# Kernel tuning notes

Hardware: AMD Instinct MI355X
Metric: run time of the kernel (lower is better)

Reference implementation:

```python
import jax, jax.numpy as jnp
import numpy as np

B, LS, LL = 1024, 128, 2048
E, VOCAB = 16, 160000
NH, KD = 8, 6
LSH_DIM, TOPK = 16, 48
D_ITEM = 3 * E  # 48
EPS = 1e-3  # keras LayerNormalization default epsilon


def setup_inputs() -> dict:
    key = jax.random.key(0)
    ks = iter(jax.random.split(key, 64))
    def nk():
        return next(ks)
    def ids(shape):
        return jax.random.randint(nk(), shape, 0, VOCAB, dtype=jnp.int32)
    inp = {}
    for n in ['uid', 'utag1', 'utag2', 'utag3', 'utag4',
              'label_goods_ids', 'label_shop_ids', 'label_cate_ids']:
        inp[n] = ids((B,))
    for n in ['shortterm_goods_ids', 'shortterm_shop_ids', 'shortterm_cate_ids']:
        inp[n] = ids((B, LS))
    for n in ['longterm_goods_ids', 'longterm_shop_ids', 'longterm_cate_ids']:
        inp[n] = ids((B, LL))
    def rn(shape, s=0.05):
        return (jax.random.normal(nk(), shape) * s).astype(jnp.float32)
    inp['emb_table'] = rn((VOCAB, E))
    inp['H'] = rn((D_ITEM, LSH_DIM), 1.0)  # non-trainable random projection
    for p in ('s', 'l'):
        inp[p + 'Wq'] = rn((D_ITEM, NH, KD)); inp[p + 'bq'] = jnp.zeros((NH, KD), jnp.float32)
        inp[p + 'Wk'] = rn((D_ITEM, NH, KD)); inp[p + 'bk'] = jnp.zeros((NH, KD), jnp.float32)
        inp[p + 'Wv'] = rn((D_ITEM, NH, KD)); inp[p + 'bv'] = jnp.zeros((NH, KD), jnp.float32)
        inp[p + 'Wo'] = rn((NH, KD, D_ITEM)); inp[p + 'bo'] = jnp.zeros((D_ITEM,), jnp.float32)
    Din = D_ITEM + 5 * E + D_ITEM + D_ITEM  # 224
    inp['W1'] = rn((Din, 200)); inp['b1'] = jnp.zeros((200,), jnp.float32)
    inp['g1'] = jnp.ones((200,), jnp.float32); inp['be1'] = jnp.zeros((200,), jnp.float32)
    inp['W2'] = rn((200, 80)); inp['b2'] = jnp.zeros((80,), jnp.float32)
    inp['g2'] = jnp.ones((80,), jnp.float32); inp['be2'] = jnp.zeros((80,), jnp.float32)
    inp['W3'] = rn((80, 1)); inp['b3'] = jnp.zeros((1,), jnp.float32)
    return inp


def _ln(x, g, b):
    m = jnp.mean(x, axis=-1, keepdims=True)
    v = jnp.mean((x - m) ** 2, axis=-1, keepdims=True)
    return (x - m) * jax.lax.rsqrt(v + EPS) * g + b


def _mha(q, kv, mask3, Wq, bq, Wk, bk, Wv, bv, Wo, bo):
    # q: [B,1,D], kv: [B,K,D], mask3: [B,1,K] float (1=keep)
    qh = jnp.einsum('bqe,ehd->bqhd', q, Wq) + bq
    kh = jnp.einsum('bke,ehd->bkhd', kv, Wk) + bk
    vh = jnp.einsum('bke,ehd->bkhd', kv, Wv) + bv
    sc = jnp.einsum('bqhd,bkhd->bhqk', qh, kh) / jnp.sqrt(jnp.float32(KD))
    sc = sc + (1.0 - mask3[:, None, :, :]) * jnp.float32(-1e9)
    a = jax.nn.softmax(sc, axis=-1)
    o = jnp.einsum('bhqk,bkhd->bqhd', a, vh)
    return jnp.einsum('bqhd,hde->bqe', o, Wo) + bo


def reference(uid, utag1, utag2, utag3, utag4,
              label_goods_ids, label_shop_ids, label_cate_ids,
              shortterm_goods_ids, shortterm_shop_ids, shortterm_cate_ids,
              longterm_goods_ids, longterm_shop_ids, longterm_cate_ids,
              emb_table, H,
              sWq, sbq, sWk, sbk, sWv, sbv, sWo, sbo,
              lWq, lbq, lWk, lbk, lWv, lbv, lWo, lbo,
              W1, b1, g1, be1, W2, b2, g2, be2, W3, b3):
    short_mask = shortterm_goods_ids == 0  # padding_index == 0
    long_mask = longterm_goods_ids == 0

    def stack_embed(lst):
        X = jnp.stack([t if t.ndim == 2 else t[:, None] for t in lst], axis=2)  # [B,L,F]
        Xe = emb_table[X]  # [B,L,F,E]
        return Xe.reshape(Xe.shape[0], Xe.shape[1], -1)

    X_item = stack_embed([label_goods_ids, label_shop_ids, label_cate_ids])  # [B,1,48]
    X_user = stack_embed([uid, utag1, utag2, utag3, utag4])                  # [B,1,80]
    X_short = stack_embed([shortterm_goods_ids, shortterm_shop_ids, shortterm_cate_ids])  # [B,LS,48]
    X_long = stack_embed([longterm_goods_ids, longterm_shop_ids, longterm_cate_ids])      # [B,LL,48]

    # short-term interest
    slen = jnp.sum((~short_mask).astype(jnp.int32), axis=1)
    smask = (jnp.arange(LS)[None, :] < slen[:, None]).astype(jnp.float32)[:, None, :]
    short_int = _mha(X_item, X_short, smask, sWq, sbq, sWk, sbk, sWv, sbv, sWo, sbo)[:, 0]

    # long-term interest: LSH sign-hash hamming top-k retrieval
    series_codes = jnp.sign(jnp.einsum('ble,em->blm', X_long, H))  # [B,LL,16]
    item_codes = jnp.sign(jnp.einsum('ble,em->blm', X_item, H))    # [B,1,16]
    scores = jnp.sum((series_codes == item_codes).astype(jnp.float32), axis=-1)  # [B,LL]
    scores = jnp.where(long_mask, -jnp.inf, scores)
    _, idx = jax.lax.top_k(scores, TOPK)  # descending, padded entries last
    top_emb = jnp.take_along_axis(X_long, idx[:, :, None], axis=1)  # [B,TOPK,48]
    top_mask = jnp.take_along_axis(long_mask, idx, axis=1)
    llen = jnp.sum((~top_mask).astype(jnp.int32), axis=1)
    lmask = (jnp.arange(TOPK)[None, :] < llen[:, None]).astype(jnp.float32)[:, None, :]
    long_int = _mha(X_item, top_emb, lmask, lWq, lbq, lWk, lbk, lWv, lbv, lWo, lbo)[:, 0]

    x = jnp.concatenate([X_item[:, 0], X_user[:, 0], short_int, long_int], axis=1)  # [B,224]
    h1 = jax.nn.relu(_ln(x @ W1 + b1, g1, be1))
    h2 = jax.nn.relu(_ln(h1 @ W2 + b2, g2, be2))
    out = jax.nn.sigmoid(h2 @ W3 + b3)  # [B,1]
    return out
```

## Files before the change

### kernel.cpp

```cpp
#include <hip/hip_runtime.h>
#include <math.h>

#define BB 1024
#define LSx 128
#define LLx 2048
#define TOPKx 48

__global__ __launch_bounds__(256) void k_score_topk(
    const int* __restrict__ lg, const int* __restrict__ lsh, const int* __restrict__ lc,
    const int* __restrict__ ig, const int* __restrict__ ish, const int* __restrict__ ici,
    const float* __restrict__ emb, const float* __restrict__ Hm,
    int* __restrict__ sel)
{
  __shared__ float Xitem[48];
  __shared__ int icode[16];
  __shared__ signed char scores[LLx];
  __shared__ int hist[18];
  __shared__ int cnt_above;
  __shared__ int wsum[4];
  const int b = blockIdx.x, tid = threadIdx.x;

  if (tid < 48) {
    const int seg = tid >> 4, e = tid & 15;
    const int id = (seg == 0) ? ig[b] : (seg == 1) ? ish[b] : ici[b];
    Xitem[tid] = emb[(size_t)id * 16 + e];
  }
  if (tid < 18) hist[tid] = 0;
  if (tid == 0) cnt_above = 0;
  __syncthreads();
  if (tid < 16) {
    float dd = 0.f;
    for (int e = 0; e < 48; ++e) dd += Xitem[e] * Hm[e * 16 + tid];
    icode[tid] = (dd > 0.f) ? 1 : (dd < 0.f ? -1 : 0);
  }
  __syncthreads();

  for (int j = 0; j < LLx / 256; ++j) {
    const int l = j * 256 + tid;
    const size_t off = (size_t)b * LLx + l;
    const int gid = lg[off];
    int sc;
    if (gid == 0) {
      sc = -1;
    } else {
      const int sid = lsh[off], cid = lc[off];
      float d[16];
      #pragma unroll
      for (int m = 0; m < 16; ++m) d[m] = 0.f;
      const int ids3[3] = {gid, sid, cid};
      #pragma unroll
      for (int seg = 0; seg < 3; ++seg) {
        const float* row = emb + (size_t)ids3[seg] * 16;
        const float4 r0 = ((const float4*)row)[0];
        const float4 r1 = ((const float4*)row)[1];
        const float4 r2 = ((const float4*)row)[2];
        const float4 r3 = ((const float4*)row)[3];
        const float x[16] = {r0.x, r0.y, r0.z, r0.w, r1.x, r1.y, r1.z, r1.w,
                             r2.x, r2.y, r2.z, r2.w, r3.x, r3.y, r3.z, r3.w};
        const float* hb = Hm + seg * 256;
        #pragma unroll
        for (int i = 0; i < 16; ++i) {
          const float xi = x[i];
          #pragma unroll
          for (int mc = 0; mc < 4; ++mc) {
            const float4 h4 = *(const float4*)(hb + i * 16 + mc * 4);
            d[mc * 4 + 0] += xi * h4.x;
            d[mc * 4 + 1] += xi * h4.y;
            d[mc * 4 + 2] += xi * h4.z;
            d[mc * 4 + 3] += xi * h4.w;
          }
        }
      }
      sc = 0;
      #pragma unroll
      for (int m = 0; m < 16; ++m) {
        const int cs = (d[m] > 0.f) ? 1 : (d[m] < 0.f ? -1 : 0);
        sc += (cs == icode[m]) ? 1 : 0;
      }
    }
    scores[l] = (signed char)sc;
    atomicAdd(&hist[sc + 1], 1);
  }
  __syncthreads();

  int above = 0, tval = -1, need = 0;
  for (int s = 16; s >= -1; --s) {
    const int c = hist[s + 1];
    if (above + c >= TOPKx) { tval = s; need = TOPKx - above; break; }
    above += c;
  }

  const int base_l = tid * (LLx / 256);
  int cnt = 0;
  for (int j = 0; j < LLx / 256; ++j) cnt += (scores[base_l + j] == tval) ? 1 : 0;
  int v = cnt;
  const int lane = tid & 63, wave = tid >> 6;
  #pragma unroll
  for (int o = 1; o < 64; o <<= 1) {
    const int u = __shfl_up(v, o, 64);
    if (lane >= o) v += u;
  }
  if (lane == 63) wsum[wave] = v;
  __syncthreads();
  int rank = v - cnt;
  for (int w = 0; w < wave; ++w) rank += wsum[w];

  for (int j = 0; j < LLx / 256; ++j) {
    const int l = base_l + j;
    const int s = scores[l];
    if (s > tval) {
      const int slot = atomicAdd(&cnt_above, 1);
      sel[b * TOPKx + slot] = l;
    } else if (s == tval) {
      if (rank < need) sel[b * TOPKx + above + rank] = l;
      ++rank;
    }
  }
}

template<int K, int STRIDE, bool IS_LONG>
__global__ __launch_bounds__(128) void k_mha(
    const int* __restrict__ kg, const int* __restrict__ ks, const int* __restrict__ kc,
    const int* __restrict__ ig, const int* __restrict__ ish, const int* __restrict__ ici,
    const float* __restrict__ emb,
    const float* __restrict__ Wq, const float* __restrict__ bq,
    const float* __restrict__ Wk, const float* __restrict__ bk,
    const float* __restrict__ Wv, const float* __restrict__ bv,
    const float* __restrict__ Wo, const float* __restrict__ bo,
    const int* __restrict__ sel,
    float* __restrict__ outv)
{
  __shared__ float Xitem[48];
  __shared__ float qh[48];
  __shared__ __align__(16) float vhs[K][48];
  __shared__ float scs[8][K + 4];
  __shared__ float osm[48];
  __shared__ unsigned char validf[K];
  const int b = blockIdx.x, tid = threadIdx.x;

  if (tid < 48) {
    const int seg = tid >> 4, e = tid & 15;
    const int id = (seg == 0) ? ig[b] : (seg == 1) ? ish[b] : ici[b];
    Xitem[tid] = emb[(size_t)id * 16 + e];
  }
  __syncthreads();
  if (tid < 48) {
    float a = bq[tid];
    for (int e = 0; e < 48; ++e) a += Xitem[e] * Wq[e * 48 + tid];
    qh[tid] = a;
  }

  int gid = 0, sid = 0, cid = 0;
  if (tid < K) {
    const int pos = IS_LONG ? sel[b * TOPKx + tid] : tid;
    const size_t off = (size_t)b * STRIDE + pos;
    gid = kg[off]; sid = ks[off]; cid = kc[off];
  }
  const int nval = __syncthreads_count((tid < K) && (gid != 0));

  if (tid < K) {
    validf[tid] = IS_LONG ? (unsigned char)(gid != 0) : (unsigned char)(tid < nval);
    float kh[48], vh[48];
    #pragma unroll
    for (int j = 0; j < 48; ++j) { kh[j] = bk[j]; vh[j] = bv[j]; }
    const int ids3[3] = {gid, sid, cid};
    #pragma unroll
    for (int seg = 0; seg < 3; ++seg) {
      const float* row = emb + (size_t)ids3[seg] * 16;
      #pragma unroll
      for (int i4 = 0; i4 < 4; ++i4) {
        const float4 xv = ((const float4*)row)[i4];
        const float xs[4] = {xv.x, xv.y, xv.z, xv.w};
        #pragma unroll
        for (int c = 0; c < 4; ++c) {
          const int e = seg * 16 + i4 * 4 + c;
          const float* wkr = Wk + e * 48;
          const float* wvr = Wv + e * 48;
          const float xe = xs[c];
          #pragma unroll
          for (int j = 0; j < 48; ++j) {
            kh[j] += xe * wkr[j];
            vh[j] += xe * wvr[j];
          }
        }
      }
    }
    #pragma unroll
    for (int h = 0; h < 8; ++h) {
      float s = 0.f;
      #pragma unroll
      for (int d = 0; d < 6; ++d) s += qh[h * 6 + d] * kh[h * 6 + d];
      scs[h][tid] = s * 0.40824829046386301637f;
    }
    #pragma unroll
    for (int j = 0; j < 48; ++j) vhs[tid][j] = vh[j];
  }
  __syncthreads();

  {
    const int h = tid >> 4, l16 = tid & 15;
    float amax = -INFINITY;
    for (int k = l16; k < K; k += 16) if (validf[k]) amax = fmaxf(amax, scs[h][k]);
    #pragma unroll
    for (int m = 1; m < 16; m <<= 1) amax = fmaxf(amax, __shfl_xor(amax, m, 16));
    if (nval == 0) {
      for (int k = l16; k < K; k += 16) scs[h][k] = 1.0f / (float)K;
    } else {
      float ssum = 0.f;
      for (int k = l16; k < K; k += 16) {
        const float ev = validf[k] ? expf(scs[h][k] - amax) : 0.f;
        scs[h][k] = ev;
        ssum += ev;
      }
      #pragma unroll
      for (int m = 1; m < 16; m <<= 1) ssum += __shfl_xor(ssum, m, 16);
      const float inv = 1.0f / ssum;
      for (int k = l16; k < K; k += 16) scs[h][k] *= inv;
    }
  }
  __syncthreads();

  if (tid < 48) {
    const int h = tid / 6;
    float a = 0.f;
    for (int k = 0; k < K; ++k) a += scs[h][k] * vhs[k][tid];
    osm[tid] = a;
  }
  __syncthreads();
  if (tid < 48) {
    float r = bo[tid];
    for (int j = 0; j < 48; ++j) r += osm[j] * Wo[j * 48 + tid];
    outv[b * 48 + tid] = r;
  }
}

__device__ __forceinline__ float block_sum256(float v, float* red) {
  #pragma unroll
  for (int m = 32; m >= 1; m >>= 1) v += __shfl_xor(v, m, 64);
  const int lane = threadIdx.x & 63, wave = threadIdx.x >> 6;
  if (lane == 0) red[wave] = v;
  __syncthreads();
  const float t = red[0] + red[1] + red[2] + red[3];
  __syncthreads();
  return t;
}

__global__ __launch_bounds__(256) void k_mlp(
    const int* __restrict__ uid, const int* __restrict__ u1, const int* __restrict__ u2,
    const int* __restrict__ u3, const int* __restrict__ u4,
    const int* __restrict__ ig, const int* __restrict__ ish, const int* __restrict__ ici,
    const float* __restrict__ emb,
    const float* __restrict__ sint, const float* __restrict__ lint,
    const float* __restrict__ W1, const float* __restrict__ b1,
    const float* __restrict__ g1, const float* __restrict__ be1,
    const float* __restrict__ W2, const float* __restrict__ b2,
    const float* __restrict__ g2, const float* __restrict__ be2,
    const float* __restrict__ W3, const float* __restrict__ b3,
    float* __restrict__ out)
{
  __shared__ __align__(16) float x[224];
  __shared__ __align__(16) float h1[200];
  __shared__ float h2[80];
  __shared__ float red[4];
  const int b = blockIdx.x, tid = threadIdx.x;

  if (tid < 128) {
    const int e = tid & 15;
    int id;
    if (tid < 48) {
      const int seg = tid >> 4;
      id = (seg == 0) ? ig[b] : (seg == 1) ? ish[b] : ici[b];
    } else {
      const int f = (tid - 48) >> 4;
      id = (f == 0) ? uid[b] : (f == 1) ? u1[b] : (f == 2) ? u2[b] : (f == 3) ? u3[b] : u4[b];
    }
    x[tid] = emb[(size_t)id * 16 + e];
  } else if (tid < 176) {
    x[tid] = sint[b * 48 + (tid - 128)];
  } else if (tid < 224) {
    x[tid] = lint[b * 48 + (tid - 176)];
  }
  __syncthreads();

  float v = 0.f;
  if (tid < 200) {
    v = b1[tid];
    for (int i4 = 0; i4 < 56; ++i4) {
      const float4 xv = *(const float4*)(x + i4 * 4);
      const float* w = W1 + i4 * 4 * 200 + tid;
      v += xv.x * w[0];
      v += xv.y * w[200];
      v += xv.z * w[400];
      v += xv.w * w[600];
    }
  }
  const float mean1 = block_sum256((tid < 200) ? v : 0.f, red) * (1.0f / 200.0f);
  const float dv = (tid < 200) ? (v - mean1) : 0.f;
  const float var1 = block_sum256(dv * dv, red) * (1.0f / 200.0f);
  if (tid < 200) {
    const float y = (v - mean1) * rsqrtf(var1 + 1e-3f) * g1[tid] + be1[tid];
    h1[tid] = fmaxf(y, 0.f);
  }
  __syncthreads();

  float v2 = 0.f;
  if (tid < 80) {
    v2 = b2[tid];
    for (int i4 = 0; i4 < 50; ++i4) {
      const float4 xv = *(const float4*)(h1 + i4 * 4);
      const float* w = W2 + i4 * 4 * 80 + tid;
      v2 += xv.x * w[0];
      v2 += xv.y * w[80];
      v2 += xv.z * w[160];
      v2 += xv.w * w[240];
    }
  }
  const float mean2 = block_sum256((tid < 80) ? v2 : 0.f, red) * (1.0f / 80.0f);
  const float dv2 = (tid < 80) ? (v2 - mean2) : 0.f;
  const float var2 = block_sum256(dv2 * dv2, red) * (1.0f / 80.0f);
  if (tid < 80) {
    const float y = (v2 - mean2) * rsqrtf(var2 + 1e-3f) * g2[tid] + be2[tid];
    h2[tid] = fmaxf(y, 0.f);
  }
  __syncthreads();

  const float p = (tid < 80) ? h2[tid] * W3[tid] : 0.f;
  const float z = block_sum256(p, red);
  if (tid == 0) {
    out[b] = 1.0f / (1.0f + expf(-(z + b3[0])));
  }
}

extern "C" void kernel_launch(void* const* d_in, const int* in_sizes, int n_in,
                              void* d_out, int out_size, void* d_ws, size_t ws_size,
                              hipStream_t stream) {
  (void)in_sizes; (void)n_in; (void)out_size; (void)ws_size;
  const int* uid = (const int*)d_in[0];
  const int* u1  = (const int*)d_in[1];
  const int* u2  = (const int*)d_in[2];
  const int* u3  = (const int*)d_in[3];
  const int* u4  = (const int*)d_in[4];
  const int* ig  = (const int*)d_in[5];
  const int* ish = (const int*)d_in[6];
  const int* ici = (const int*)d_in[7];
  const int* sg  = (const int*)d_in[8];
  const int* ss  = (const int*)d_in[9];
  const int* scd = (const int*)d_in[10];
  const int* lg  = (const int*)d_in[11];
  const int* ls  = (const int*)d_in[12];
  const int* lcd = (const int*)d_in[13];
  const float* emb = (const float*)d_in[14];
  const float* Hm  = (const float*)d_in[15];
  const float* sWq = (const float*)d_in[16];
  const float* sbq = (const float*)d_in[17];
  const float* sWk = (const float*)d_in[18];
  const float* sbk = (const float*)d_in[19];
  const float* sWv = (const float*)d_in[20];
  const float* sbv = (const float*)d_in[21];
  const float* sWo = (const float*)d_in[22];
  const float* sbo = (const float*)d_in[23];
  const float* lWq = (const float*)d_in[24];
  const float* lbq = (const float*)d_in[25];
  const float* lWk = (const float*)d_in[26];
  const float* lbk = (const float*)d_in[27];
  const float* lWv = (const float*)d_in[28];
  const float* lbv = (const float*)d_in[29];
  const float* lWo = (const float*)d_in[30];
  const float* lbo = (const float*)d_in[31];
  const float* W1 = (const float*)d_in[32];
  const float* b1 = (const float*)d_in[33];
  const float* g1 = (const float*)d_in[34];
  const float* be1 = (const float*)d_in[35];
  const float* W2 = (const float*)d_in[36];
  const float* b2 = (const float*)d_in[37];
  const float* g2 = (const float*)d_in[38];
  const float* be2 = (const float*)d_in[39];
  const float* W3 = (const float*)d_in[40];
  const float* b3 = (const float*)d_in[41];
  float* out = (float*)d_out;

  int* sel = (int*)d_ws;
  float* sint = (float*)d_ws + BB * TOPKx;
  float* lint = sint + BB * 48;

  k_score_topk<<<dim3(BB), dim3(256), 0, stream>>>(lg, ls, lcd, ig, ish, ici, emb, Hm, sel);
  k_mha<128, 128, false><<<dim3(BB), dim3(128), 0, stream>>>(
      sg, ss, scd, ig, ish, ici, emb,
      sWq, sbq, sWk, sbk, sWv, sbv, sWo, sbo, (const int*)nullptr, sint);
  k_mha<48, 2048, true><<<dim3(BB), dim3(128), 0, stream>>>(
      lg, ls, lcd, ig, ish, ici, emb,
      lWq, lbq, lWk, lbk, lWv, lbv, lWo, lbo, sel, lint);
  k_mlp<<<dim3(BB), dim3(256), 0, stream>>>(
      uid, u1, u2, u3, u4, ig, ish, ici, emb,
      sint, lint, W1, b1, g1, be1, W2, b2, g2, be2, W3, b3, out);
}
```

Baseline: 337.0 us.

## Split LSH scoring across more blocks and fuse top-k into long MHA

The scoring kernel now launches one block per 256 sequence positions per batch row (8x more blocks), each thread scoring a single position and writing int8 scores to global workspace. Top-k selection (histogram threshold, prefix-rank tie handling) moves into a new long-attention kernel that keeps the selected indices in shared memory and then runs the attention directly. This aims to raise occupancy and parallelism in the gather-heavy scoring stage and to avoid writing and rereading the selected indices. In exchange, each scoring block recomputes the item code, and the scores take a 2MB round trip through global memory.

New measurement: 352.4 us. +4.6%, slower.

```diff
diff --git a/kernel.cpp b/kernel.cpp
--- a/kernel.cpp
+++ b/kernel.cpp
@@ -6,27 +6,21 @@
 #define LLx 2048
 #define TOPKx 48
 
-__global__ __launch_bounds__(256) void k_score_topk(
+__global__ __launch_bounds__(256) void k_score(
     const int* __restrict__ lg, const int* __restrict__ lsh, const int* __restrict__ lc,
     const int* __restrict__ ig, const int* __restrict__ ish, const int* __restrict__ ici,
     const float* __restrict__ emb, const float* __restrict__ Hm,
-    int* __restrict__ sel)
+    signed char* __restrict__ gsc)
 {
   __shared__ float Xitem[48];
   __shared__ int icode[16];
-  __shared__ signed char scores[LLx];
-  __shared__ int hist[18];
-  __shared__ int cnt_above;
-  __shared__ int wsum[4];
-  const int b = blockIdx.x, tid = threadIdx.x;
+  const int b = blockIdx.y, tid = threadIdx.x;
 
   if (tid < 48) {
     const int seg = tid >> 4, e = tid & 15;
     const int id = (seg == 0) ? ig[b] : (seg == 1) ? ish[b] : ici[b];
     Xitem[tid] = emb[(size_t)id * 16 + e];
   }
-  if (tid < 18) hist[tid] = 0;
-  if (tid == 0) cnt_above = 0;
   __syncthreads();
   if (tid < 16) {
     float dd = 0.f;
@@ -35,87 +29,49 @@
   }
   __syncthreads();
 
-  for (int j = 0; j < LLx / 256; ++j) {
-    const int l = j * 256 + tid;
-    const size_t off = (size_t)b * LLx + l;
-    const int gid = lg[off];
-    int sc;
-    if (gid == 0) {
-      sc = -1;
-    } else {
-      const int sid = lsh[off], cid = lc[off];
-      float d[16];
-      #pragma unroll
-      for (int m = 0; m < 16; ++m) d[m] = 0.f;
-      const int ids3[3] = {gid, sid, cid};
-      #pragma unroll
-      for (int seg = 0; seg < 3; ++seg) {
-        const float* row = emb + (size_t)ids3[seg] * 16;
-        const float4 r0 = ((const float4*)row)[0];
-        const float4 r1 = ((const float4*)row)[1];
-        const float4 r2 = ((const float4*)row)[2];
-        const float4 r3 = ((const float4*)row)[3];
-        const float x[16] = {r0.x, r0.y, r0.z, r0.w, r1.x, r1.y, r1.z, r1.w,
-                             r2.x, r2.y, r2.z, r2.w, r3.x, r3.y, r3.z, r3.w};
-        const float* hb = Hm + seg * 256;
+  const int l = blockIdx.x * 256 + tid;
+  const size_t off = (size_t)b * LLx + l;
+  const int gid = lg[off];
+  int sc;
+  if (gid == 0) {
+    sc = -1;
+  } else {
+    const int sid = lsh[off], cid = lc[off];
+    float d[16];
+    #pragma unroll
+    for (int m = 0; m < 16; ++m) d[m] = 0.f;
+    const int ids3[3] = {gid, sid, cid};
+    #pragma unroll
+    for (int seg = 0; seg < 3; ++seg) {
+      const float* row = emb + (size_t)ids3[seg] * 16;
+      const float4 r0 = ((const float4*)row)[0];
+      const float4 r1 = ((const float4*)row)[1];
+      const float4 r2 = ((const float4*)row)[2];
+      const float4 r3 = ((const float4*)row)[3];
+      const float x[16] = {r0.x, r0.y, r0.z, r0.w, r1.x, r1.y, r1.z, r1.w,
+                           r2.x, r2.y, r2.z, r2.w, r3.x, r3.y, r3.z, r3.w};
+      const float* hb = Hm + seg * 256;
+      #pragma unroll
+      for (int i = 0; i < 16; ++i) {
+        const float xi = x[i];
         #pragma unroll
-        for (int i = 0; i < 16; ++i) {
-          const float xi = x[i];
-          #pragma unroll
-          for (int mc = 0; mc < 4; ++mc) {
-            const float4 h4 = *(const float4*)(hb + i * 16 + mc * 4);
-            d[mc * 4 + 0] += xi * h4.x;
-            d[mc * 4 + 1] += xi * h4.y;
-            d[mc * 4 + 2] += xi * h4.z;
-            d[mc * 4 + 3] += xi * h4.w;
-          }
+        for (int mc = 0; mc < 4; ++mc) {
+          const float4 h4 = *(const float4*)(hb + i * 16 + mc * 4);
+          d[mc * 4 + 0] += xi * h4.x;
+          d[mc * 4 + 1] += xi * h4.y;
+          d[mc * 4 + 2] += xi * h4.z;
+          d[mc * 4 + 3] += xi * h4.w;
         }
       }
-      sc = 0;
-      #pragma unroll
-      for (int m = 0; m < 16; ++m) {
-        const int cs = (d[m] > 0.f) ? 1 : (d[m] < 0.f ? -1 : 0);
-        sc += (cs == icode[m]) ? 1 : 0;
-      }
-    }
-    scores[l] = (signed char)sc;
-    atomicAdd(&hist[sc + 1], 1);
-  }
-  __syncthreads();
-
-  int above = 0, tval = -1, need = 0;
-  for (int s = 16; s >= -1; --s) {
-    const int c = hist[s + 1];
-    if (above + c >= TOPKx) { tval = s; need = TOPKx - above; break; }
-    above += c;
-  }
-
-  const int base_l = tid * (LLx / 256);
-  int cnt = 0;
-  for (int j = 0; j < LLx / 256; ++j) cnt += (scores[base_l + j] == tval) ? 1 : 0;
-  int v = cnt;
-  const int lane = tid & 63, wave = tid >> 6;
-  #pragma unroll
-  for (int o = 1; o < 64; o <<= 1) {
-    const int u = __shfl_up(v, o, 64);
-    if (lane >= o) v += u;
-  }
-  if (lane == 63) wsum[wave] = v;
-  __syncthreads();
-  int rank = v - cnt;
-  for (int w = 0; w < wave; ++w) rank += wsum[w];
-
-  for (int j = 0; j < LLx / 256; ++j) {
-    const int l = base_l + j;
-    const int s = scores[l];
-    if (s > tval) {
-      const int slot = atomicAdd(&cnt_above, 1);
-      sel[b * TOPKx + slot] = l;
-    } else if (s == tval) {
-      if (rank < need) sel[b * TOPKx + above + rank] = l;
-      ++rank;
-    }
-  }
+    }
+    sc = 0;
+    #pragma unroll
+    for (int m = 0; m < 16; ++m) {
+      const int cs = (d[m] > 0.f) ? 1 : (d[m] < 0.f ? -1 : 0);
+      sc += (cs == icode[m]) ? 1 : 0;
+    }
+  }
+  gsc[off] = (signed char)sc;
 }
 
 template<int K, int STRIDE, bool IS_LONG>
@@ -224,6 +180,172 @@
     const int h = tid / 6;
     float a = 0.f;
     for (int k = 0; k < K; ++k) a += scs[h][k] * vhs[k][tid];
+    osm[tid] = a;
+  }
+  __syncthreads();
+  if (tid < 48) {
+    float r = bo[tid];
+    for (int j = 0; j < 48; ++j) r += osm[j] * Wo[j * 48 + tid];
+    outv[b * 48 + tid] = r;
+  }
+}
+
+__global__ __launch_bounds__(256) void k_mha_long(
+    const int* __restrict__ kg, const int* __restrict__ ks, const int* __restrict__ kc,
+    const int* __restrict__ ig, const int* __restrict__ ish, const int* __restrict__ ici,
+    const float* __restrict__ emb,
+    const float* __restrict__ Wq, const float* __restrict__ bq,
+    const float* __restrict__ Wk, const float* __restrict__ bk,
+    const float* __restrict__ Wv, const float* __restrict__ bv,
+    const float* __restrict__ Wo, const float* __restrict__ bo,
+    const signed char* __restrict__ gsc,
+    float* __restrict__ outv)
+{
+  __shared__ int hist[18];
+  __shared__ int cnt_above;
+  __shared__ int wsum[4];
+  __shared__ int selsh[TOPKx];
+  __shared__ float Xitem[48];
+  __shared__ float qh[48];
+  __shared__ __align__(16) float vhs[TOPKx][48];
+  __shared__ float scs[8][TOPKx + 4];
+  __shared__ float osm[48];
+  __shared__ unsigned char validf[TOPKx];
+  const int b = blockIdx.x, tid = threadIdx.x;
+
+  const int2 myv = ((const int2*)(gsc + (size_t)b * LLx))[tid];
+  signed char loc[8];
+  *(int2*)loc = myv;
+
+  if (tid < 18) hist[tid] = 0;
+  if (tid == 0) cnt_above = 0;
+  if (tid < 48) {
+    const int seg = tid >> 4, e = tid & 15;
+    const int id = (seg == 0) ? ig[b] : (seg == 1) ? ish[b] : ici[b];
+    Xitem[tid] = emb[(size_t)id * 16 + e];
+  }
+  __syncthreads();
+
+  #pragma unroll
+  for (int j = 0; j < 8; ++j) atomicAdd(&hist[(int)loc[j] + 1], 1);
+  if (tid < 48) {
+    float a = bq[tid];
+    for (int e = 0; e < 48; ++e) a += Xitem[e] * Wq[e * 48 + tid];
+    qh[tid] = a;
+  }
+  __syncthreads();
+
+  int above = 0, tval = -1, need = 0;
+  for (int s = 16; s >= -1; --s) {
+    const int c = hist[s + 1];
+    if (above + c >= TOPKx) { tval = s; need = TOPKx - above; break; }
+    above += c;
+  }
+
+  const int base_l = tid * (LLx / 256);
+  int cnt = 0;
+  #pragma unroll
+  for (int j = 0; j < 8; ++j) cnt += ((int)loc[j] == tval) ? 1 : 0;
+  int v = cnt;
+  const int lane = tid & 63, wave = tid >> 6;
+  #pragma unroll
+  for (int o = 1; o < 64; o <<= 1) {
+    const int u = __shfl_up(v, o, 64);
+    if (lane >= o) v += u;
+  }
+  if (lane == 63) wsum[wave] = v;
+  __syncthreads();
+  int rank = v - cnt;
+  for (int w = 0; w < wave; ++w) rank += wsum[w];
+
+  #pragma unroll
+  for (int j = 0; j < 8; ++j) {
+    const int l = base_l + j;
+    const int s = (int)loc[j];
+    if (s > tval) {
+      const int slot = atomicAdd(&cnt_above, 1);
+      selsh[slot] = l;
+    } else if (s == tval) {
+      if (rank < need) selsh[above + rank] = l;
+      ++rank;
+    }
+  }
+  __syncthreads();
+
+  int gid = 0, sid = 0, cid = 0;
+  if (tid < TOPKx) {
+    const int pos = selsh[tid];
+    const size_t off = (size_t)b * LLx + pos;
+    gid = kg[off]; sid = ks[off]; cid = kc[off];
+  }
+  const int nval = __syncthreads_count((tid < TOPKx) && (gid != 0));
+
+  if (tid < TOPKx) {
+    validf[tid] = (unsigned char)(gid != 0);
+    float kh[48], vh[48];
+    #pragma unroll
+    for (int j = 0; j < 48; ++j) { kh[j] = bk[j]; vh[j] = bv[j]; }
+    const int ids3[3] = {gid, sid, cid};
+    #pragma unroll
+    for (int seg = 0; seg < 3; ++seg) {
+      const float* row = emb + (size_t)ids3[seg] * 16;
+      #pragma unroll
+      for (int i4 = 0; i4 < 4; ++i4) {
+        const float4 xv = ((const float4*)row)[i4];
+        const float xs[4] = {xv.x, xv.y, xv.z, xv.w};
+        #pragma unroll
+        for (int c = 0; c < 4; ++c) {
+          const int e = seg * 16 + i4 * 4 + c;
+          const float* wkr = Wk + e * 48;
+          const float* wvr = Wv + e * 48;
+          const float xe = xs[c];
+          #pragma unroll
+          for (int j = 0; j < 48; ++j) {
+            kh[j] += xe * wkr[j];
+            vh[j] += xe * wvr[j];
+          }
+        }
+      }
+    }
+    #pragma unroll
+    for (int h = 0; h < 8; ++h) {
+      float s = 0.f;
+      #pragma unroll
+      for (int d = 0; d < 6; ++d) s += qh[h * 6 + d] * kh[h * 6 + d];
+      scs[h][tid] = s * 0.40824829046386301637f;
+    }
+    #pragma unroll
+    for (int j = 0; j < 48; ++j) vhs[tid][j] = vh[j];
+  }
+  __syncthreads();
+
+  if (tid < 128) {
+    const int h = tid >> 4, l16 = tid & 15;
+    float amax = -INFINITY;
+    for (int k = l16; k < TOPKx; k += 16) if (validf[k]) amax = fmaxf(amax, scs[h][k]);
+    #pragma unroll
+    for (int m = 1; m < 16; m <<= 1) amax = fmaxf(amax, __shfl_xor(amax, m, 16));
+    if (nval == 0) {
+      for (int k = l16; k < TOPKx; k += 16) scs[h][k] = 1.0f / (float)TOPKx;
+    } else {
+      float ssum = 0.f;
+      for (int k = l16; k < TOPKx; k += 16) {
+        const float ev = validf[k] ? expf(scs[h][k] - amax) : 0.f;
+        scs[h][k] = ev;
+        ssum += ev;
+      }
+      #pragma unroll
+      for (int m = 1; m < 16; m <<= 1) ssum += __shfl_xor(ssum, m, 16);
+      const float inv = 1.0f / ssum;
+      for (int k = l16; k < TOPKx; k += 16) scs[h][k] *= inv;
+    }
+  }
+  __syncthreads();
+
+  if (tid < 48) {
+    const int h = tid / 6;
+    float a = 0.f;
+    for (int k = 0; k < TOPKx; ++k) a += scs[h][k] * vhs[k][tid];
     osm[tid] = a;
   }
   __syncthreads();
@@ -379,17 +501,18 @@
   const float* b3 = (const float*)d_in[41];
   float* out = (float*)d_out;
 
-  int* sel = (int*)d_ws;
-  float* sint = (float*)d_ws + BB * TOPKx;
+  signed char* gsc = (signed char*)d_ws;
+  float* sint = (float*)((char*)d_ws + (size_t)BB * LLx);
   float* lint = sint + BB * 48;
 
-  k_score_topk<<<dim3(BB), dim3(256), 0, stream>>>(lg, ls, lcd, ig, ish, ici, emb, Hm, sel);
+  k_score<<<dim3(LLx / 256, BB), dim3(256), 0, stream>>>(
+      lg, ls, lcd, ig, ish, ici, emb, Hm, gsc);
   k_mha<128, 128, false><<<dim3(BB), dim3(128), 0, stream>>>(
       sg, ss, scd, ig, ish, ici, emb,
       sWq, sbq, sWk, sbk, sWv, sbv, sWo, sbo, (const int*)nullptr, sint);
-  k_mha<48, 2048, true><<<dim3(BB), dim3(128), 0, stream>>>(
+  k_mha_long<<<dim3(BB), dim3(256), 0, stream>>>(
       lg, ls, lcd, ig, ish, ici, emb,
-      lWq, lbq, lWk, lbk, lWv, lbv, lWo, lbo, sel, lint);
+      lWq, lbq, lWk, lbk, lWv, lbv, lWo, lbo, gsc, lint);
   k_mlp<<<dim3(BB), dim3(256), 0, stream>>>(
       uid, u1, u2, u3, u4, ig, ish, ici, emb,
       sint, lint, W1, b1, g1, be1, W2, b2, g2, be2, W3, b3, out);
```

## Split LSH scoring into a wide grid kernel and a separate top-k kernel

Applied to the files above, without the earlier changes.

Scoring of long-term items moves into its own kernel launched over (LL/256, B) blocks, so each thread scores one item instead of looping over eight, and scores go to a global int8 buffer. Embedding rows are gathered cooperatively, with four threads per row loading float4s into shared memory so the reads coalesce. A separate top-k kernel reads the scores back with one int2 per thread and runs the histogram and selection on registers. This exposes more parallelism to hide gather latency, at the cost of an extra launch and a global round trip for the scores.

New measurement: 327.9 us. -2.7%, faster.

```diff
diff --git a/kernel.cpp b/kernel.cpp
--- a/kernel.cpp
+++ b/kernel.cpp
@@ -6,81 +6,106 @@
 #define LLx 2048
 #define TOPKx 48
 
-__global__ __launch_bounds__(256) void k_score_topk(
+__global__ __launch_bounds__(256, 2) void k_score(
     const int* __restrict__ lg, const int* __restrict__ lsh, const int* __restrict__ lc,
     const int* __restrict__ ig, const int* __restrict__ ish, const int* __restrict__ ici,
     const float* __restrict__ emb, const float* __restrict__ Hm,
-    int* __restrict__ sel)
+    signed char* __restrict__ gsc)
 {
   __shared__ float Xitem[48];
   __shared__ int icode[16];
-  __shared__ signed char scores[LLx];
+  __shared__ __align__(16) float4 xsh[256][5];
+  const int b = blockIdx.y, tid = threadIdx.x;
+
+  const int l = blockIdx.x * 256 + tid;
+  const size_t off = (size_t)b * LLx + l;
+  const int gid = lg[off];
+
+  if (tid < 48) {
+    const int seg = tid >> 4, e = tid & 15;
+    const int id = (seg == 0) ? ig[b] : (seg == 1) ? ish[b] : ici[b];
+    Xitem[tid] = emb[(size_t)id * 16 + e];
+  }
+  __syncthreads();
+  if (tid < 16) {
+    float dd = 0.f;
+    for (int e = 0; e < 48; ++e) dd += Xitem[e] * Hm[e * 16 + tid];
+    icode[tid] = (dd > 0.f) ? 1 : (dd < 0.f ? -1 : 0);
+  }
+
+  const int srow = tid >> 2;
+  const int q = tid & 3;
+  const size_t bbase = (size_t)b * LLx + (size_t)blockIdx.x * 256;
+
+  float d[16];
+  #pragma unroll
+  for (int m = 0; m < 16; ++m) d[m] = 0.f;
+
+  #pragma unroll
+  for (int seg = 0; seg < 3; ++seg) {
+    const int* idarr = (seg == 0) ? lg : (seg == 1) ? lsh : lc;
+    #pragma unroll
+    for (int jj = 0; jj < 4; ++jj) {
+      const int pos = jj * 64 + srow;
+      const int id = idarr[bbase + pos];
+      xsh[pos][q] = *(const float4*)(emb + (size_t)id * 16 + q * 4);
+    }
+    __syncthreads();
+    if (gid != 0) {
+      float x[16];
+      #pragma unroll
+      for (int qq = 0; qq < 4; ++qq) {
+        const float4 r = xsh[tid][qq];
+        x[qq * 4 + 0] = r.x; x[qq * 4 + 1] = r.y;
+        x[qq * 4 + 2] = r.z; x[qq * 4 + 3] = r.w;
+      }
+      const float* hb = Hm + seg * 256;
+      #pragma unroll
+      for (int i = 0; i < 16; ++i) {
+        const float xi = x[i];
+        #pragma unroll
+        for (int mc = 0; mc < 4; ++mc) {
+          const float4 h4 = *(const float4*)(hb + i * 16 + mc * 4);
+          d[mc * 4 + 0] += xi * h4.x;
+          d[mc * 4 + 1] += xi * h4.y;
+          d[mc * 4 + 2] += xi * h4.z;
+          d[mc * 4 + 3] += xi * h4.w;
+        }
+      }
+    }
+    if (seg < 2) __syncthreads();
+  }
+
+  int sc = -1;
+  if (gid != 0) {
+    sc = 0;
+    #pragma unroll
+    for (int m = 0; m < 16; ++m) {
+      const int cs = (d[m] > 0.f) ? 1 : (d[m] < 0.f ? -1 : 0);
+      sc += (cs == icode[m]) ? 1 : 0;
+    }
+  }
+  gsc[off] = (signed char)sc;
+}
+
+__global__ __launch_bounds__(256) void k_topk(
+    const signed char* __restrict__ gsc, int* __restrict__ sel)
+{
   __shared__ int hist[18];
   __shared__ int cnt_above;
   __shared__ int wsum[4];
   const int b = blockIdx.x, tid = threadIdx.x;
 
-  if (tid < 48) {
-    const int seg = tid >> 4, e = tid & 15;
-    const int id = (seg == 0) ? ig[b] : (seg == 1) ? ish[b] : ici[b];
-    Xitem[tid] = emb[(size_t)id * 16 + e];
-  }
+  const int2 myv = ((const int2*)(gsc + (size_t)b * LLx))[tid];
+  signed char loc[8];
+  *(int2*)loc = myv;
+
   if (tid < 18) hist[tid] = 0;
   if (tid == 0) cnt_above = 0;
   __syncthreads();
-  if (tid < 16) {
-    float dd = 0.f;
-    for (int e = 0; e < 48; ++e) dd += Xitem[e] * Hm[e * 16 + tid];
-    icode[tid] = (dd > 0.f) ? 1 : (dd < 0.f ? -1 : 0);
-  }
-  __syncthreads();
-
-  for (int j = 0; j < LLx / 256; ++j) {
-    const int l = j * 256 + tid;
-    const size_t off = (size_t)b * LLx + l;
-    const int gid = lg[off];
-    int sc;
-    if (gid == 0) {
-      sc = -1;
-    } else {
-      const int sid = lsh[off], cid = lc[off];
-      float d[16];
-      #pragma unroll
-      for (int m = 0; m < 16; ++m) d[m] = 0.f;
-      const int ids3[3] = {gid, sid, cid};
-      #pragma unroll
-      for (int seg = 0; seg < 3; ++seg) {
-        const float* row = emb + (size_t)ids3[seg] * 16;
-        const float4 r0 = ((const float4*)row)[0];
-        const float4 r1 = ((const float4*)row)[1];
-        const float4 r2 = ((const float4*)row)[2];
-        const float4 r3 = ((const float4*)row)[3];
-        const float x[16] = {r0.x, r0.y, r0.z, r0.w, r1.x, r1.y, r1.z, r1.w,
-                             r2.x, r2.y, r2.z, r2.w, r3.x, r3.y, r3.z, r3.w};
-        const float* hb = Hm + seg * 256;
-        #pragma unroll
-        for (int i = 0; i < 16; ++i) {
-          const float xi = x[i];
-          #pragma unroll
-          for (int mc = 0; mc < 4; ++mc) {
-            const float4 h4 = *(const float4*)(hb + i * 16 + mc * 4);
-            d[mc * 4 + 0] += xi * h4.x;
-            d[mc * 4 + 1] += xi * h4.y;
-            d[mc * 4 + 2] += xi * h4.z;
-            d[mc * 4 + 3] += xi * h4.w;
-          }
-        }
-      }
-      sc = 0;
-      #pragma unroll
-      for (int m = 0; m < 16; ++m) {
-        const int cs = (d[m] > 0.f) ? 1 : (d[m] < 0.f ? -1 : 0);
-        sc += (cs == icode[m]) ? 1 : 0;
-      }
-    }
-    scores[l] = (signed char)sc;
-    atomicAdd(&hist[sc + 1], 1);
-  }
+
+  #pragma unroll
+  for (int j = 0; j < 8; ++j) atomicAdd(&hist[(int)loc[j] + 1], 1);
   __syncthreads();
 
   int above = 0, tval = -1, need = 0;
@@ -92,7 +117,8 @@
 
   const int base_l = tid * (LLx / 256);
   int cnt = 0;
-  for (int j = 0; j < LLx / 256; ++j) cnt += (scores[base_l + j] == tval) ? 1 : 0;
+  #pragma unroll
+  for (int j = 0; j < 8; ++j) cnt += ((int)loc[j] == tval) ? 1 : 0;
   int v = cnt;
   const int lane = tid & 63, wave = tid >> 6;
   #pragma unroll
@@ -105,9 +131,10 @@
   int rank = v - cnt;
   for (int w = 0; w < wave; ++w) rank += wsum[w];
 
-  for (int j = 0; j < LLx / 256; ++j) {
+  #pragma unroll
+  for (int j = 0; j < 8; ++j) {
     const int l = base_l + j;
-    const int s = scores[l];
+    const int s = (int)loc[j];
     if (s > tval) {
       const int slot = atomicAdd(&cnt_above, 1);
       sel[b * TOPKx + slot] = l;
@@ -379,11 +406,14 @@
   const float* b3 = (const float*)d_in[41];
   float* out = (float*)d_out;
 
-  int* sel = (int*)d_ws;
-  float* sint = (float*)d_ws + BB * TOPKx;
+  signed char* gsc = (signed char*)d_ws;
+  int* sel = (int*)((char*)d_ws + (size_t)BB * LLx);
+  float* sint = (float*)(sel + BB * TOPKx);
   float* lint = sint + BB * 48;
 
-  k_score_topk<<<dim3(BB), dim3(256), 0, stream>>>(lg, ls, lcd, ig, ish, ici, emb, Hm, sel);
+  k_score<<<dim3(LLx / 256, BB), dim3(256), 0, stream>>>(
+      lg, ls, lcd, ig, ish, ici, emb, Hm, gsc);
+  k_topk<<<dim3(BB), dim3(256), 0, stream>>>(gsc, sel);
   k_mha<128, 128, false><<<dim3(BB), dim3(128), 0, stream>>>(
       sg, ss, scd, ig, ish, ici, emb,
       sWq, sbq, sWk, sbk, sWv, sbv, sWo, sbo, (const int*)nullptr, sint);
```
